# Performance work log

Measured on AMD Instinct MI355X. Metric: run time of the kernel, lower is better.

The kernel has to match this reference:

```python
import jax, jax.numpy as jnp
from jax import lax
import numpy as np

# Module config (from init_kwargs / torch defaults)
CONF_THRES = 0.25
IOU_THRES = 0.45
MAX_DET = 300          # torch non_max_suppression max_det
BATCH = 16
N_PRED = 25200         # YOLOv5 anchors @ 640x640
NC = 80                # COCO classes
IMG = 640.0


def setup_inputs() -> dict:
    key = jax.random.key(0)
    k1, k2 = jax.random.split(key)
    # raw YOLO head output: [xywh (pixels), obj in [0,1], 80 class probs in [0,1]]
    prediction = jax.random.uniform(k1, (BATCH, N_PRED, NC + 5), dtype=jnp.float32)
    prediction = prediction.at[:, :, :4].multiply(IMG)  # realistic pixel-scale boxes
    logits = jax.random.normal(k2, (BATCH, N_PRED, NC), dtype=jnp.float32)
    return {"prediction": prediction, "logits": logits}


def _xywh2xyxy(x):
    xy, wh = x[..., :2], x[..., 2:4]
    return jnp.concatenate([xy - wh * 0.5, xy + wh * 0.5], axis=-1)


def _nms_image(pred, logit):
    """pred: [N, 85], logit: [N, 80] -> [MAX_DET, 87] padded detections.

    Row layout: [x1, y1, x2, y2, conf, cls, objectness, logits(80)].
    Invalid (padding) rows are zeroed, matching the variable-length torch output.
    """
    obj = pred[:, 4]                              # [N]
    cls_conf = pred[:, 5:] * obj[:, None]         # conf = cls_prob * obj  [N, 80]
    conf = jnp.max(cls_conf, axis=1)              # best-class confidence
    cls = jnp.argmax(cls_conf, axis=1)
    boxes = _xywh2xyxy(pred[:, :4])               # [N, 4] xyxy
    # candidate mask: obj > conf_thres (xc) AND best conf > conf_thres (conf_mask)
    valid = (obj > CONF_THRES) & (conf > CONF_THRES)
    scores0 = jnp.where(valid, conf, -jnp.inf)
    area = (boxes[:, 2] - boxes[:, 0]) * (boxes[:, 3] - boxes[:, 1])  # [N]

    # agnostic NMS (agnostic_nms=True -> no per-class box offset)
    def step(sc, _):
        idx = jnp.argmax(sc)                      # highest remaining score
        ok = jnp.isfinite(sc[idx])                # any candidate left?
        b = boxes[idx]
        lt = jnp.maximum(b[:2], boxes[:, :2])
        rb = jnp.minimum(b[2:], boxes[:, 2:])
        wh = jnp.clip(rb - lt, 0.0)
        inter = wh[:, 0] * wh[:, 1]
        iou = inter / (area[idx] + area - inter + 1e-9)
        sc = jnp.where(iou > IOU_THRES, -jnp.inf, sc)  # suppress (incl. self)
        return sc, (idx, ok)

    _, (sel, ok) = lax.scan(step, scores0, None, length=MAX_DET)

    det = jnp.concatenate(
        [boxes[sel], conf[sel][:, None], cls[sel][:, None].astype(jnp.float32),
         obj[sel][:, None], logit[sel]], axis=1)  # [MAX_DET, 87]
    return det * ok[:, None].astype(det.dtype)


def reference(prediction, logits):
    # [B, MAX_DET, 87]: xyxy(4) | conf | cls | objectness | class logits(80)
    return jax.vmap(_nms_image)(prediction, logits)
```

## Files before the change

### kernel.cpp

```cpp
#include <hip/hip_runtime.h>
#include <math.h>

#define NPRED  25200
#define BATCH  16
#define NC     80
#define MAXDET 300
#define NDIM   87
#define NBIN   1024

#define WS_SC      0
#define WS_BOX     1612800
#define WS_SELIDX  8064000
#define WS_SELCNT  8083200
#define WS_HIST    8083264
#define WS_CURSOR  8148800
#define WS_IA      8214336
#define WS_BINNED  8279872

#define PREP_TPB 256
#define PB 128

__global__ __launch_bounds__(PREP_TPB)
void prep_kernel(const float* __restrict__ pred,
                 float* __restrict__ sc,
                 float4* __restrict__ box,
                 unsigned int* __restrict__ hist) {
    __shared__ float4 s4[PB * 85 / 4];
    __shared__ float sPart[PB];
    float* s = (float*)s4;
    const int t = threadIdx.x;
    const float4* p4 = (const float4*)(pred + (size_t)blockIdx.x * (PB * 85));
    for (int i = t; i < PB * 85 / 4; i += PREP_TPB) s4[i] = p4[i];
    __syncthreads();
    const int r = t & (PB - 1);
    const float* row = s + r * 85;
    const float obj = row[4];
    float part = -INFINITY;
    const int c0 = (t < PB) ? 0 : 40;
    #pragma unroll 8
    for (int c = c0; c < c0 + 40; ++c) {
        float v = __fmul_rn(row[5 + c], obj);
        if (v > part) part = v;
    }
    if (t >= PB) sPart[r] = part;
    __syncthreads();
    if (t < PB) {
        float best = fmaxf(part, sPart[r]);
        float x = row[0], y = row[1], w = row[2], h = row[3];
        float hw = __fmul_rn(w, 0.5f), hh = __fmul_rn(h, 0.5f);
        bool valid = (obj > 0.25f) && (best > 0.25f);
        int g = blockIdx.x * PB + t;
        sc[g]  = valid ? best : -INFINITY;
        box[g] = make_float4(__fsub_rn(x, hw), __fsub_rn(y, hh),
                             __fadd_rn(x, hw), __fadd_rn(y, hh));
        if (valid) {
            int img = g / NPRED;
            unsigned int sb = __float_as_uint(best);
            int bin = min((int)((sb - 0x3E800000u) >> 14), NBIN - 1);
            atomicAdd(&hist[img * NBIN + bin], 1u);
        }
    }
}

__global__ __launch_bounds__(NBIN)
void scan_kernel(const unsigned int* __restrict__ hist,
                 unsigned int* __restrict__ IaG,
                 unsigned int* __restrict__ cursor) {
    __shared__ unsigned int sA[NBIN], sB[NBIN];
    const int img = blockIdx.x, t = threadIdx.x;
    unsigned int cnt = hist[img * NBIN + t];
    sA[t] = cnt;
    __syncthreads();
    unsigned int *src = sA, *dst = sB;
    for (int d = 1; d < NBIN; d <<= 1) {
        dst[t] = src[t] + ((t + d) < NBIN ? src[t + d] : 0u);
        __syncthreads();
        unsigned int* tmp = src; src = dst; dst = tmp;
    }
    IaG[img * NBIN + t]    = src[t];
    cursor[img * NBIN + t] = src[t] - cnt;
}

#define SCB  16
#define STPB 512

__global__ __launch_bounds__(STPB)
void scatter_kernel(const float* __restrict__ sc,
                    unsigned int* __restrict__ cursor,
                    unsigned long long* __restrict__ binned) {
    const int img = blockIdx.x / SCB, part = blockIdx.x % SCB;
    const float* sci = sc + (size_t)img * NPRED;
    for (int e = part * STPB + threadIdx.x; e < NPRED; e += SCB * STPB) {
        float s = sci[e];
        if (s != -INFINITY) {
            unsigned int sb = __float_as_uint(s);
            int bin = min((int)((sb - 0x3E800000u) >> 14), NBIN - 1);
            unsigned int pos = atomicAdd(&cursor[img * NBIN + bin], 1u);
            binned[(size_t)img * NPRED + pos] =
                ((unsigned long long)(~sb) << 32) | (unsigned int)e;
        }
    }
}

#define BS_TPB 256
#define BS_CAP 4096

__global__ __launch_bounds__(BS_TPB)
void binsort_kernel(const unsigned int* __restrict__ hist,
                    const unsigned int* __restrict__ IaG,
                    unsigned long long* __restrict__ binned) {
    __shared__ unsigned long long lds[BS_CAP];
    const int img = blockIdx.x >> 10, b = blockIdx.x & (NBIN - 1);
    const int t = threadIdx.x;
    const int cnt = (int)hist[img * NBIN + b];
    if (cnt <= 1) return;
    const int start = (int)IaG[img * NBIN + b] - cnt;
    unsigned long long* ptr = binned + (size_t)img * NPRED + start;

    if (cnt <= 64) {
        if (t < 64) {
            unsigned long long key = (t < cnt) ? ptr[t] : ~0ULL;
            #pragma unroll
            for (int k = 2; k <= 64; k <<= 1) {
                #pragma unroll
                for (int j = k >> 1; j > 0; j >>= 1) {
                    unsigned long long other = __shfl_xor(key, j);
                    bool up = ((t & k) == 0), lower = ((t & j) == 0);
                    unsigned long long mn = min(key, other), mx = max(key, other);
                    key = (up == lower) ? mn : mx;
                }
            }
            if (t < cnt) ptr[t] = key;
        }
        return;
    }
    const int cap = min(cnt, BS_CAP);
    int m = 64; while (m < cap) m <<= 1;
    for (int i = t; i < m; i += BS_TPB) lds[i] = (i < cap) ? ptr[i] : ~0ULL;
    __syncthreads();
    for (int k = 2; k <= m; k <<= 1) {
        for (int j = k >> 1; j > 0; j >>= 1) {
            for (int i = t; i < m; i += BS_TPB) {
                int l = i ^ j;
                if (l > i) {
                    unsigned long long a = lds[i], b2 = lds[l];
                    if ((a > b2) == ((i & k) == 0)) { lds[i] = b2; lds[l] = a; }
                }
            }
            __syncthreads();
        }
    }
    for (int i = t; i < cap; i += BS_TPB) ptr[i] = lds[i];
}

#define TPB      1024
#define TCAP     4096
#define FIRSTCAP 1024
#define SLOTS    4
#define NW       (TPB / 64)

__device__ __forceinline__ bool iou_gt(float Bx1, float By1, float Bx2, float By2,
                                       float BA,
                                       float cx1, float cy1, float cx2, float cy2,
                                       float ca, double K) {
    float lx = fmaxf(Bx1, cx1), ly = fmaxf(By1, cy1);
    float rx = fminf(Bx2, cx2), ry = fminf(By2, cy2);
    float ww = fmaxf(__fsub_rn(rx, lx), 0.0f);
    float hh = fmaxf(__fsub_rn(ry, ly), 0.0f);
    float inter = __fmul_rn(ww, hh);
    float denom = __fadd_rn(__fsub_rn(__fadd_rn(BA, ca), inter), 1e-9f);
    return ((double)inter > K * (double)denom);
}

__device__ __forceinline__ int blk_min(int v, int* s_red, int t, int wid) {
    __syncthreads();
    #pragma unroll
    for (int off = 32; off; off >>= 1) v = min(v, __shfl_down(v, off));
    if ((t & 63) == 0) s_red[wid] = v;
    __syncthreads();
    int r = s_red[0];
    #pragma unroll
    for (int w = 1; w < NW; ++w) r = min(r, s_red[w]);
    return r;
}

__global__ __launch_bounds__(TPB)
void nms_kernel(const unsigned long long* __restrict__ binned,
                const unsigned int* __restrict__ IaG,
                const float4* __restrict__ box_g,
                int* __restrict__ selidx,
                int* __restrict__ selcnt) {
    __shared__ unsigned long long sbuf[TCAP];
    __shared__ unsigned int IaL[NBIN];
    __shared__ float4 kbox[MAXDET];
    __shared__ float  karea[MAXDET];
    __shared__ unsigned char s_alive[TCAP];
    __shared__ int s_red[NW];
    __shared__ unsigned int s_wsum[NW];
    __shared__ int s_kept, s_sticky, s_stickyIdx, s_fillFrom;

    const int img = blockIdx.x, t = threadIdx.x, wid = t >> 6, lane = t & 63;
    const float4* bxi = box_g + (size_t)img * NPRED;
    const unsigned long long* bin_img = binned + (size_t)img * NPRED;
    const double K = (double)0.45f + 0x1p-26;

    IaL[t] = IaG[img * NBIN + t];
    if (t == 0) { s_kept = 0; s_sticky = 0; }
    __syncthreads();
    const int n_valid = (int)IaL[0];

    int o = 0, b_hi = NBIN;
    bool firstT = true;
    for (;;) {
        __syncthreads();
        if (s_kept >= MAXDET || s_sticky || o >= n_valid) break;

        const int cap = firstT ? FIRSTCAP : TCAP;
        int vb = (t < b_hi && ((int)IaL[t] - o) <= cap) ? t : 0x7FFFFFFF;
        int b_lo = blk_min(vb, s_red, t, wid);
        if (b_lo == 0x7FFFFFFF && cap != TCAP) {
            vb = (t < b_hi && ((int)IaL[t] - o) <= TCAP) ? t : 0x7FFFFFFF;
            b_lo = blk_min(vb, s_red, t, wid);
        }
        int c;
        if (b_lo != 0x7FFFFFFF) {
            c = (int)IaL[b_lo] - o;
        } else {
            vb = (t < b_hi && ((int)IaL[t] - o) > 0) ? -t : 0x7FFFFFFF;
            int m2 = blk_min(vb, s_red, t, wid);
            b_lo = -m2;
            c = min((int)IaL[b_lo] - o, TCAP);
        }
        if (c <= 0) break;

        const int kept0 = s_kept;

        const int S = (c + 1023) >> 10;
        unsigned int um = 0;
        unsigned long long ukey[SLOTS];
        {
            float ux1[SLOTS], uy1[SLOTS], ux2[SLOTS], uy2[SLOTS], uar[SLOTS];
            #pragma unroll
            for (int s = 0; s < SLOTS; ++s) {
                int p = wid * (S << 6) + (s << 6) + lane;
                bool av = (s < S) && (p < c);
                unsigned long long key = av ? bin_img[o + p] : ~0ULL;
                ukey[s] = key;
                unsigned int ix = av ? (unsigned int)key : 0u;
                float4 b = bxi[ix];
                ux1[s] = b.x; uy1[s] = b.y; ux2[s] = b.z; uy2[s] = b.w;
                uar[s] = __fmul_rn(__fsub_rn(b.z, b.x), __fsub_rn(b.w, b.y));
                if (av) um |= (1u << s);
            }
            if (kept0 > 0 && um) {
                for (int kb = 0; kb < kept0 && um; kb += 4) {
                    float4 Bc[4]; float Ac[4];
                    #pragma unroll
                    for (int i = 0; i < 4; ++i) {
                        int j = kb + i; j = (j < kept0) ? j : kept0 - 1;
                        Bc[i] = kbox[j]; Ac[i] = karea[j];
                    }
                    #pragma unroll
                    for (int i = 0; i < 4; ++i) {
                        #pragma unroll
                        for (int s = 0; s < SLOTS; ++s) {
                            if (um & (1u << s)) {
                                if (iou_gt(Bc[i].x, Bc[i].y, Bc[i].z, Bc[i].w, Ac[i],
                                           ux1[s], uy1[s], ux2[s], uy2[s], uar[s], K))
                                    um &= ~(1u << s);
                            }
                        }
                    }
                }
            }
        }
        int myoff[SLOTS];
        unsigned int wcnt = 0;
        const unsigned long long lt = (lane == 0) ? 0ULL : (~0ULL >> (64 - lane));
        #pragma unroll
        for (int s = 0; s < SLOTS; ++s) {
            unsigned long long bal = __ballot((int)((um >> s) & 1u));
            myoff[s] = (int)(wcnt + __popcll(bal & lt));
            wcnt += (unsigned int)__popcll(bal);
        }
        if (lane == 0) s_wsum[wid] = wcnt;
        __syncthreads();
        int wbase = 0, cnt2 = 0;
        #pragma unroll
        for (int w = 0; w < NW; ++w) {
            int v = (int)s_wsum[w];
            if (w < wid) wbase += v;
            cnt2 += v;
        }
        #pragma unroll
        for (int s = 0; s < SLOTS; ++s)
            if (um & (1u << s)) sbuf[wbase + myoff[s]] = ukey[s];
        __syncthreads();

        if (cnt2 > 0) {
            unsigned int rm = 0;
            float rx1[SLOTS], ry1[SLOTS], rx2[SLOTS], ry2[SLOTS], rar[SLOTS];
            #pragma unroll
            for (int s = 0; s < SLOTS; ++s) {
                int p = t * SLOTS + s;
                bool av = (p < cnt2);
                unsigned int ix = av ? (unsigned int)sbuf[p] : 0u;
                float4 b = bxi[ix];
                rx1[s] = b.x; ry1[s] = b.y; rx2[s] = b.z; ry2[s] = b.w;
                rar[s] = __fmul_rn(__fsub_rn(b.z, b.x), __fsub_rn(b.w, b.y));
                if (av) rm |= (1u << s);
                s_alive[p] = av ? 1 : 0;
            }
            __syncthreads();

            const int nwin = (cnt2 + 63) >> 6;
            int applied = kept0;
            for (int g = 0; g < nwin; ++g) {
                int k0 = s_kept;
                if (rm) {
                    for (int kb = applied; kb < k0 && rm; kb += 4) {
                        float4 Bc[4]; float Ac[4];
                        #pragma unroll
                        for (int i = 0; i < 4; ++i) {
                            int j = kb + i; j = (j < k0) ? j : k0 - 1;
                            Bc[i] = kbox[j]; Ac[i] = karea[j];
                        }
                        #pragma unroll
                        for (int i = 0; i < 4; ++i) {
                            #pragma unroll
                            for (int s = 0; s < SLOTS; ++s) {
                                if (rm & (1u << s)) {
                                    if (iou_gt(Bc[i].x, Bc[i].y, Bc[i].z, Bc[i].w, Ac[i],
                                               rx1[s], ry1[s], rx2[s], ry2[s], rar[s], K)) {
                                        rm &= ~(1u << s);
                                        s_alive[t * SLOTS + s] = 0;
                                    }
                                }
                            }
                        }
                    }
                }
                applied = k0;
                __syncthreads();
                if (t < 64) {
                    int p = g * 64 + t;
                    int a = s_alive[p];
                    unsigned int ix = a ? (unsigned int)sbuf[p] : 0u;
                    float4 b = bxi[ix];
                    float cx1 = b.x, cy1 = b.y, cx2 = b.z, cy2 = b.w;
                    float car = __fmul_rn(__fsub_rn(b.z, b.x), __fsub_rn(b.w, b.y));
                    int kept = k0;
                    for (;;) {
                        unsigned long long bal = __ballot(a != 0);
                        if (!bal) break;
                        int f = (int)__builtin_ctzll(bal);
                        float Bx1 = __shfl(cx1, f), By1 = __shfl(cy1, f);
                        float Bx2 = __shfl(cx2, f), By2 = __shfl(cy2, f);
                        float BA  = __shfl(car, f);
                        int bidx  = __shfl((int)ix, f);
                        if (t == f) a = 0;
                        if (t == 0) {
                            selidx[img * MAXDET + kept] = bidx;
                            kbox[kept] = make_float4(Bx1, By1, Bx2, By2);
                            karea[kept] = BA;
                        }
                        float dns = __fadd_rn(__fsub_rn(__fadd_rn(BA, BA), BA), 1e-9f);
                        if (!((double)BA > K * (double)dns)) {
                            if (t == 0) { s_sticky = 1; s_stickyIdx = bidx; s_fillFrom = kept + 1; }
                            kept = MAXDET;
                            break;
                        }
                        if (a) {
                            if (iou_gt(Bx1, By1, Bx2, By2, BA,
                                       cx1, cy1, cx2, cy2, car, K)) a = 0;
                        }
                        ++kept;
                        if (kept >= MAXDET) break;
                    }
                    if (t == 0) s_kept = kept;
                }
                __syncthreads();
                if (((t * SLOTS) >> 6) == g) rm = 0;
                if (s_kept >= MAXDET || s_sticky) break;
            }
        }
        o += c;
        if (o >= (int)IaL[b_lo]) b_hi = b_lo;
        firstT = false;
    }
    int keptF = s_kept;
    if (s_sticky) {
        for (int k2 = s_fillFrom + t; k2 < MAXDET; k2 += TPB)
            selidx[img * MAXDET + k2] = s_stickyIdx;
        keptF = MAXDET;
    }
    if (t == 0) selcnt[img] = keptF;
}

#define GT 256

__global__ __launch_bounds__(GT)
void gather_kernel(const float* __restrict__ pred,
                   const float4* __restrict__ box,
                   const float* __restrict__ logits,
                   const int* __restrict__ selidx,
                   const int* __restrict__ selcnt,
                   float* __restrict__ out) {
    int tid = blockIdx.x * GT + threadIdx.x;
    if (tid >= BATCH * MAXDET * NDIM) return;
    int row = tid / NDIM, col = tid - row * NDIM;
    int img = row / MAXDET, det = row - img * MAXDET;
    float v = 0.0f;
    if (det < selcnt[img]) {
        int s = selidx[img * MAXDET + det];
        size_t g = (size_t)img * NPRED + s;
        if (col < 4) {
            float4 b = box[g];
            v = (col == 0) ? b.x : (col == 1) ? b.y : (col == 2) ? b.z : b.w;
        } else if (col == 6) {
            v = pred[g * 85 + 4];
        } else if (col >= 7) {
            v = logits[g * NC + (col - 7)];
        } else {
            const float* p = pred + g * 85;
            float obj = p[4];
            float best = -INFINITY; int bc = 0;
            #pragma unroll 8
            for (int c = 0; c < NC; ++c) {
                float q = __fmul_rn(p[5 + c], obj);
                if (q > best) { best = q; bc = c; }
            }
            v = (col == 4) ? best : (float)bc;
        }
    }
    out[tid] = v;
}

extern "C" void kernel_launch(void* const* d_in, const int* in_sizes, int n_in,
                              void* d_out, int out_size, void* d_ws, size_t ws_size,
                              hipStream_t stream) {
    const float* pred   = (const float*)d_in[0];
    const float* logits = (const float*)d_in[1];
    float* out = (float*)d_out;

    char* ws = (char*)d_ws;
    float*              sc     = (float*)(ws + WS_SC);
    float4*             box    = (float4*)(ws + WS_BOX);
    int*                selidx = (int*)(ws + WS_SELIDX);
    int*                selcnt = (int*)(ws + WS_SELCNT);
    unsigned int*       hist   = (unsigned int*)(ws + WS_HIST);
    unsigned int*       cursor = (unsigned int*)(ws + WS_CURSOR);
    unsigned int*       IaG    = (unsigned int*)(ws + WS_IA);
    unsigned long long* binned = (unsigned long long*)(ws + WS_BINNED);

    hipMemsetAsync(hist, 0, BATCH * NBIN * sizeof(unsigned int), stream);

    prep_kernel<<<BATCH * NPRED / PB, PREP_TPB, 0, stream>>>(pred, sc, box, hist);
    scan_kernel<<<BATCH, NBIN, 0, stream>>>(hist, IaG, cursor);
    scatter_kernel<<<BATCH * SCB, STPB, 0, stream>>>(sc, cursor, binned);
    binsort_kernel<<<BATCH * NBIN, BS_TPB, 0, stream>>>(hist, IaG, binned);
    nms_kernel<<<BATCH, TPB, 0, stream>>>(binned, IaG, box, selidx, selcnt);
    int gtot = BATCH * MAXDET * NDIM;
    gather_kernel<<<(gtot + GT - 1) / GT, GT, 0, stream>>>(pred, box, logits, selidx, selcnt, out);
}
```

Baseline: 290.6 us.

## Process NMS windows per-wave with register-resident candidates and shrink binsort blocks

Result: slower. 343.0 us (+18.0%).

```diff
diff --git a/kernel.cpp b/kernel.cpp
--- a/kernel.cpp
+++ b/kernel.cpp
@@ -102,8 +102,8 @@
     }
 }
 
-#define BS_TPB 256
-#define BS_CAP 4096
+#define BS_TPB 64
+#define BS_CAP 1024
 
 __global__ __launch_bounds__(BS_TPB)
 void binsort_kernel(const unsigned int* __restrict__ hist,
@@ -118,20 +118,18 @@
     unsigned long long* ptr = binned + (size_t)img * NPRED + start;
 
     if (cnt <= 64) {
-        if (t < 64) {
-            unsigned long long key = (t < cnt) ? ptr[t] : ~0ULL;
+        unsigned long long key = (t < cnt) ? ptr[t] : ~0ULL;
+        #pragma unroll
+        for (int k = 2; k <= 64; k <<= 1) {
             #pragma unroll
-            for (int k = 2; k <= 64; k <<= 1) {
-                #pragma unroll
-                for (int j = k >> 1; j > 0; j >>= 1) {
-                    unsigned long long other = __shfl_xor(key, j);
-                    bool up = ((t & k) == 0), lower = ((t & j) == 0);
-                    unsigned long long mn = min(key, other), mx = max(key, other);
-                    key = (up == lower) ? mn : mx;
-                }
-            }
-            if (t < cnt) ptr[t] = key;
-        }
+            for (int j = k >> 1; j > 0; j >>= 1) {
+                unsigned long long other = __shfl_xor(key, j);
+                bool up = ((t & k) == 0), lower = ((t & j) == 0);
+                unsigned long long mn = min(key, other), mx = max(key, other);
+                key = (up == lower) ? mn : mx;
+            }
+        }
+        if (t < cnt) ptr[t] = key;
         return;
     }
     const int cap = min(cnt, BS_CAP);
@@ -158,6 +156,7 @@
 #define FIRSTCAP 1024
 #define SLOTS    4
 #define NW       (TPB / 64)
+#define WWIN     (SLOTS * 64)
 
 __device__ __forceinline__ bool iou_gt(float Bx1, float By1, float Bx2, float By2,
                                        float BA,
@@ -194,7 +193,6 @@
     __shared__ unsigned int IaL[NBIN];
     __shared__ float4 kbox[MAXDET];
     __shared__ float  karea[MAXDET];
-    __shared__ unsigned char s_alive[TCAP];
     __shared__ int s_red[NW];
     __shared__ unsigned int s_wsum[NW];
     __shared__ int s_kept, s_sticky, s_stickyIdx, s_fillFrom;
@@ -299,25 +297,26 @@
 
         if (cnt2 > 0) {
             unsigned int rm = 0;
+            unsigned int rIdx[SLOTS];
             float rx1[SLOTS], ry1[SLOTS], rx2[SLOTS], ry2[SLOTS], rar[SLOTS];
             #pragma unroll
             for (int s = 0; s < SLOTS; ++s) {
-                int p = t * SLOTS + s;
+                int p = wid * WWIN + (s << 6) + lane;
                 bool av = (p < cnt2);
                 unsigned int ix = av ? (unsigned int)sbuf[p] : 0u;
+                rIdx[s] = ix;
                 float4 b = bxi[ix];
                 rx1[s] = b.x; ry1[s] = b.y; rx2[s] = b.z; ry2[s] = b.w;
                 rar[s] = __fmul_rn(__fsub_rn(b.z, b.x), __fsub_rn(b.w, b.y));
                 if (av) rm |= (1u << s);
-                s_alive[p] = av ? 1 : 0;
             }
             __syncthreads();
 
-            const int nwin = (cnt2 + 63) >> 6;
+            const int nwin = (cnt2 + WWIN - 1) / WWIN;
             int applied = kept0;
             for (int g = 0; g < nwin; ++g) {
-                int k0 = s_kept;
-                if (rm) {
+                const int k0 = s_kept;
+                if (rm && k0 > applied) {
                     for (int kb = applied; kb < k0 && rm; kb += 4) {
                         float4 Bc[4]; float Ac[4];
                         #pragma unroll
@@ -331,56 +330,57 @@
                             for (int s = 0; s < SLOTS; ++s) {
                                 if (rm & (1u << s)) {
                                     if (iou_gt(Bc[i].x, Bc[i].y, Bc[i].z, Bc[i].w, Ac[i],
-                                               rx1[s], ry1[s], rx2[s], ry2[s], rar[s], K)) {
+                                               rx1[s], ry1[s], rx2[s], ry2[s], rar[s], K))
                                         rm &= ~(1u << s);
-                                        s_alive[t * SLOTS + s] = 0;
-                                    }
                                 }
                             }
                         }
                     }
                 }
                 applied = k0;
-                __syncthreads();
-                if (t < 64) {
-                    int p = g * 64 + t;
-                    int a = s_alive[p];
-                    unsigned int ix = a ? (unsigned int)sbuf[p] : 0u;
-                    float4 b = bxi[ix];
-                    float cx1 = b.x, cy1 = b.y, cx2 = b.z, cy2 = b.w;
-                    float car = __fmul_rn(__fsub_rn(b.z, b.x), __fsub_rn(b.w, b.y));
+                if (wid == g) {
                     int kept = k0;
                     for (;;) {
-                        unsigned long long bal = __ballot(a != 0);
-                        if (!bal) break;
-                        int f = (int)__builtin_ctzll(bal);
-                        float Bx1 = __shfl(cx1, f), By1 = __shfl(cy1, f);
-                        float Bx2 = __shfl(cx2, f), By2 = __shfl(cy2, f);
-                        float BA  = __shfl(car, f);
-                        int bidx  = __shfl((int)ix, f);
-                        if (t == f) a = 0;
-                        if (t == 0) {
+                        int fs = -1, f = 0;
+                        #pragma unroll
+                        for (int s = 0; s < SLOTS; ++s) {
+                            if (fs < 0) {
+                                unsigned long long bal = __ballot((int)((rm >> s) & 1u));
+                                if (bal) { fs = s; f = (int)__builtin_ctzll(bal); }
+                            }
+                        }
+                        if (fs < 0) break;
+                        float Bx1, By1, Bx2, By2, BA; int bidx;
+                        if (fs == 0)      { Bx1=__shfl(rx1[0],f); By1=__shfl(ry1[0],f); Bx2=__shfl(rx2[0],f); By2=__shfl(ry2[0],f); BA=__shfl(rar[0],f); bidx=__shfl((int)rIdx[0],f); }
+                        else if (fs == 1) { Bx1=__shfl(rx1[1],f); By1=__shfl(ry1[1],f); Bx2=__shfl(rx2[1],f); By2=__shfl(ry2[1],f); BA=__shfl(rar[1],f); bidx=__shfl((int)rIdx[1],f); }
+                        else if (fs == 2) { Bx1=__shfl(rx1[2],f); By1=__shfl(ry1[2],f); Bx2=__shfl(rx2[2],f); By2=__shfl(ry2[2],f); BA=__shfl(rar[2],f); bidx=__shfl((int)rIdx[2],f); }
+                        else              { Bx1=__shfl(rx1[3],f); By1=__shfl(ry1[3],f); Bx2=__shfl(rx2[3],f); By2=__shfl(ry2[3],f); BA=__shfl(rar[3],f); bidx=__shfl((int)rIdx[3],f); }
+                        if (lane == f) rm &= ~(1u << fs);
+                        if (lane == 0) {
                             selidx[img * MAXDET + kept] = bidx;
                             kbox[kept] = make_float4(Bx1, By1, Bx2, By2);
                             karea[kept] = BA;
                         }
                         float dns = __fadd_rn(__fsub_rn(__fadd_rn(BA, BA), BA), 1e-9f);
                         if (!((double)BA > K * (double)dns)) {
-                            if (t == 0) { s_sticky = 1; s_stickyIdx = bidx; s_fillFrom = kept + 1; }
+                            if (lane == 0) { s_sticky = 1; s_stickyIdx = bidx; s_fillFrom = kept + 1; }
                             kept = MAXDET;
                             break;
                         }
-                        if (a) {
-                            if (iou_gt(Bx1, By1, Bx2, By2, BA,
-                                       cx1, cy1, cx2, cy2, car, K)) a = 0;
+                        #pragma unroll
+                        for (int s = 0; s < SLOTS; ++s) {
+                            if (rm & (1u << s)) {
+                                if (iou_gt(Bx1, By1, Bx2, By2, BA,
+                                           rx1[s], ry1[s], rx2[s], ry2[s], rar[s], K))
+                                    rm &= ~(1u << s);
+                            }
                         }
                         ++kept;
                         if (kept >= MAXDET) break;
                     }
-                    if (t == 0) s_kept = kept;
+                    if (lane == 0) s_kept = kept;
                 }
                 __syncthreads();
-                if (((t * SLOTS) >> 6) == g) rm = 0;
                 if (s_kept >= MAXDET || s_sticky) break;
             }
         }
```
